# Performance work log

Hardware: AMD Instinct MI355X
Metric: run time of the kernel (lower is better)

## Reference

```python
import jax, jax.numpy as jnp
import numpy as np

WS = 7            # window size
NH = 8            # num heads
C = 128           # hidden size
HS = C // NH      # head size = 16


def _rel_index(ws):
    # Swin-style relative position index for a ws x ws window -> [N, N]
    coords = np.stack(np.meshgrid(np.arange(ws), np.arange(ws), indexing='ij'), 0).reshape(2, -1)
    rel = coords[:, :, None] - coords[:, None, :] + (ws - 1)  # [2, N, N] in [0, 2ws-2]
    return jnp.asarray(rel[0] * (2 * ws - 1) + rel[1])        # [N, N] in [0, (2ws-1)^2)


def setup_inputs() -> dict:
    key = jax.random.key(0)
    ks = jax.random.split(key, 6)
    B, H, W = 16, 112, 112
    s = 0.02
    return {
        'x': jax.random.normal(ks[0], (B, H, W, C), jnp.float32),
        'w_q': jax.random.normal(ks[1], (C, C), jnp.float32) * s,
        'w_k': jax.random.normal(ks[2], (C, C), jnp.float32) * s,
        'w_v': jax.random.normal(ks[3], (C, C), jnp.float32) * s,
        'w_o': jax.random.normal(ks[4], (C, C), jnp.float32) * s,
        'b_o': jnp.zeros((C,), jnp.float32),
        'rel_bias': jax.random.normal(ks[5], ((2 * WS - 1) ** 2, NH), jnp.float32) * s,
    }


def reference(x, w_q, w_k, w_v, w_o, b_o, rel_bias):
    B, H, W, Cc = x.shape
    ws = WS
    N = ws * ws
    # window partition: [B,H,W,C] -> [B*nH*nW, ws*ws, C]
    xw = x.reshape(B, H // ws, ws, W // ws, ws, Cc)
    xw = xw.transpose(0, 1, 3, 2, 4, 5).reshape(-1, N, Cc)
    # qkv projections, split heads: [nW, N, C] -> [nW, NH, N, HS]
    scale = HS ** -0.5
    q = (xw @ w_q).reshape(-1, N, NH, HS).transpose(0, 2, 1, 3) * scale
    k = (xw @ w_k).reshape(-1, N, NH, HS).transpose(0, 2, 1, 3)
    v = (xw @ w_v).reshape(-1, N, NH, HS).transpose(0, 2, 1, 3)
    # attention logits + relative position bias
    attn = jnp.einsum('bhnd,bhmd->bhnm', q, k)
    bias = rel_bias[_rel_index(ws)].transpose(2, 0, 1)  # [NH, N, N]
    attn = jax.nn.softmax(attn + bias[None], axis=-1)
    o = jnp.einsum('bhnm,bhmd->bhnd', attn, v)
    o = o.transpose(0, 2, 1, 3).reshape(-1, N, Cc)
    o = o @ w_o + b_o
    # stitch windows back: [B*nH*nW, N, C] -> [B, H, W, C]
    o = o.reshape(B, H // ws, W // ws, ws, ws, Cc)
    return o.transpose(0, 1, 3, 2, 4, 5).reshape(B, H, W, Cc)
```

## Files before the change

kernel.cpp:

```cpp
#include <hip/hip_runtime.h>

typedef __bf16 bf16_t;
typedef __attribute__((ext_vector_type(8))) __bf16 bf16x8;
typedef __attribute__((ext_vector_type(4))) __bf16 bf16x4;
typedef __attribute__((ext_vector_type(4))) float f32x4;
typedef __attribute__((ext_vector_type(4))) short short4v;

#if __has_builtin(__builtin_amdgcn_mfma_f32_16x16x16bf16_1k)
#define HAVE_MFMA16 1
#else
#define HAVE_MFMA16 0
#endif

#if __has_builtin(__builtin_amdgcn_exp2f)
#define EXP2(x) __builtin_amdgcn_exp2f(x)
#else
#define EXP2(x) exp2f(x)
#endif

#define LDS_XW 0
#define LDS_O  0


__device__ __forceinline__ f32x4 mfma16(bf16x4 a, bf16x4 b, f32x4 c) {
#if HAVE_MFMA16
    return __builtin_amdgcn_mfma_f32_16x16x16bf16_1k(
        __builtin_bit_cast(short4v, a), __builtin_bit_cast(short4v, b), c, 0, 0, 0);
#else
    bf16x8 a8, b8;
#pragma unroll
    for (int j = 0; j < 8; ++j) { a8[j] = (bf16_t)0.0f; b8[j] = (bf16_t)0.0f; }
#pragma unroll
    for (int j = 0; j < 4; ++j) { a8[j] = a[j]; b8[j] = b[j]; }
    return __builtin_amdgcn_mfma_f32_16x16x32_bf16(a8, b8, c, 0, 0, 0);
#endif
}

__global__ void repack_kernel(const float* __restrict__ wq, const float* __restrict__ wk,
                              const float* __restrict__ wv, const float* __restrict__ wo,
                              const float* __restrict__ rel_bias, bf16_t* __restrict__ ws)
{
    const float LOG2E = 1.44269504088896f;
    int idx = blockIdx.x * 256 + threadIdx.x;
    if (idx < 65536) {
        int mat = idx >> 14;
        int r = idx & 16383;
        int j = r & 7, l = (r >> 3) & 63, nt = (r >> 9) & 7, ks = r >> 12;
        int k = ks * 32 + (l >> 4) * 8 + j;
        int n = nt * 16 + (l & 15);
        const float* w = (mat == 0) ? wq : (mat == 1) ? wk : (mat == 2) ? wv : wo;
        float v = w[k * 128 + n];
        if (mat == 0) v *= 0.25f * LOG2E;
        ws[idx] = (bf16_t)v;
    } else if (idx < 98304) {
        int r = idx - 65536;
        int h = r >> 12, m = (r >> 6) & 63, n = r & 63;
        float v = -14427.0f;
        if (m < 49 && n < 49) {
            int im = m / 7, jm = m % 7, in_ = n / 7, jn = n % 7;
            v = rel_bias[((im - in_ + 6) * 13 + (jm - jn + 6)) * 8 + h] * LOG2E;
        }
        ((float*)(ws + 65536))[r] = v;
    }
}

__global__ __launch_bounds__(512, 4)
void win_attn_kernel(const float* __restrict__ x, const float* __restrict__ b_o,
                     const bf16_t* __restrict__ wpack, float* __restrict__ out)
{
    __shared__ __align__(16) unsigned char smem[12800];
    int* offTab = (int*)(smem + 12544);
    const float* biasT = (const float*)(wpack + 65536);
    const int tid = threadIdx.x;
    const int blk = blockIdx.x;
    const int b  = blk >> 8;
    const int wh = (blk >> 4) & 15;
    const int ww = blk & 15;
    const int w  = tid >> 6;
    const int lane = tid & 63;
    const int c  = lane & 15;
    const int hi = lane >> 4;
    const f32x4 fzero = {0.f, 0.f, 0.f, 0.f};

    if (tid < 64) {
        int mm = (tid < 49) ? tid : 48;
        int i = mm / 7, j = mm - 7 * i;
        offTab[tid] = ((b * 112 + wh * 7 + i) * 112 + ww * 7 + j) * 128;
    }
#pragma unroll
    for (int it = 0; it < 4; ++it) {
        int idx = tid + it * 512;
        if (idx < 1568) {
            int m  = idx >> 5;
            int c4 = idx & 31;
            int i = m / 7, j = m - 7 * i;
            float4 v = *(const float4*)(x + ((b * 112 + wh * 7 + i) * 112 + ww * 7 + j) * 128 + c4 * 4);
            bf16x4 bv;
            bv[0] = (bf16_t)v.x; bv[1] = (bf16_t)v.y; bv[2] = (bf16_t)v.z; bv[3] = (bf16_t)v.w;
            int ch = (c4 >> 1) ^ (m & 7);
            *(bf16x4*)(smem + LDS_XW + m * 256 + ch * 16 + (c4 & 1) * 8) = bv;
        }
    }
    __syncthreads();

    bf16x4 qreg[4], kreg[4], vreg[4];
#pragma unroll
    for (int nt = 0; nt < 4; ++nt) {
        int row = nt * 16 + c;
        int rowc = (row < 49) ? row : 48;
        const unsigned char* xbase = smem + LDS_XW + rowc * 256;
        int rsw = rowc & 7;
        bf16x8 xf[4];
#pragma unroll
        for (int ks = 0; ks < 4; ++ks)
            xf[ks] = *(const bf16x8*)(xbase + (((4 * ks + hi) ^ rsw) << 4));
        f32x4 aq = fzero, ak = fzero, av = fzero;
#pragma unroll
        for (int ks = 0; ks < 4; ++ks) {
            bf16x8 w0 = *(const bf16x8*)(wpack + 0 * 16384 + ((ks * 8 + w) * 64 + lane) * 8);
            bf16x8 w1 = *(const bf16x8*)(wpack + 1 * 16384 + ((ks * 8 + w) * 64 + lane) * 8);
            bf16x8 w2 = *(const bf16x8*)(wpack + 2 * 16384 + ((ks * 8 + w) * 64 + lane) * 8);
            aq = __builtin_amdgcn_mfma_f32_16x16x32_bf16(w0, xf[ks], aq, 0, 0, 0);
            ak = __builtin_amdgcn_mfma_f32_16x16x32_bf16(w1, xf[ks], ak, 0, 0, 0);
            av = __builtin_amdgcn_mfma_f32_16x16x32_bf16(xf[ks], w2, av, 0, 0, 0);
        }
        bf16x4 q, k, vv;
#pragma unroll
        for (int r = 0; r < 4; ++r) {
            q[r]  = (bf16_t)aq[r];
            k[r]  = (bf16_t)ak[r];
            vv[r] = (bf16_t)av[r];
        }
        qreg[nt] = q; kreg[nt] = k; vreg[nt] = vv;
    }
    __syncthreads();

    const int col = 16 * w + c;
    const int colhi = col >> 3;
    const int collo = (col & 7) * 2;
    int chO[4];
#pragma unroll
    for (int r = 0; r < 4; ++r)
        chO[r] = (colhi ^ ((4 * hi + r) & 7)) * 16 + collo;
#pragma unroll
    for (int mt = 0; mt < 4; ++mt) {
        int m = mt * 16 + c;
        f32x4 st[4];
#pragma unroll
        for (int nt = 0; nt < 4; ++nt) {
            f32x4 bb = *(const f32x4*)(biasT + (w * 64 + m) * 64 + nt * 16 + 4 * hi);
            st[nt] = mfma16(kreg[nt], qreg[mt], bb);
        }
        float sum = 0.f;
#pragma unroll
        for (int nt = 0; nt < 4; ++nt)
#pragma unroll
            for (int r = 0; r < 4; ++r) {
                float p = EXP2(st[nt][r]);
                st[nt][r] = p;
                sum += p;
            }
        sum += __shfl_xor(sum, 16);
        sum += __shfl_xor(sum, 32);
        float inv = 1.f / sum;
        f32x4 oacc = fzero;
#pragma unroll
        for (int nt = 0; nt < 4; ++nt) {
            bf16x4 pv;
#pragma unroll
            for (int r = 0; r < 4; ++r) pv[r] = (bf16_t)st[nt][r];
            oacc = mfma16(pv, vreg[nt], oacc);
        }
#pragma unroll
        for (int r = 0; r < 4; ++r) {
            float invr = __shfl(inv, 4 * hi + r);
            int row = mt * 16 + hi * 4 + r;
            if (row < 49)
                *(bf16_t*)(smem + LDS_O + row * 256 + chO[r]) = (bf16_t)(oacc[r] * invr);
        }
    }
    __syncthreads();

    float bb = b_o[col];
#pragma unroll
    for (int mt = 0; mt < 4; ++mt) {
        int row = mt * 16 + c;
        int rowc = (row < 49) ? row : 48;
        f32x4 acc = fzero;
#pragma unroll
        for (int ks = 0; ks < 4; ++ks) {
            int ch = (4 * ks + hi) ^ (rowc & 7);
            bf16x8 a  = *(const bf16x8*)(smem + LDS_O + rowc * 256 + ch * 16);
            bf16x8 w0 = *(const bf16x8*)(wpack + 3 * 16384 + ((ks * 8 + w) * 64 + lane) * 8);
            acc = __builtin_amdgcn_mfma_f32_16x16x32_bf16(a, w0, acc, 0, 0, 0);
        }
        int4 o4 = *(const int4*)(offTab + mt * 16 + 4 * hi);
        int offv[4] = {o4.x, o4.y, o4.z, o4.w};
#pragma unroll
        for (int r = 0; r < 4; ++r) {
            int m = mt * 16 + hi * 4 + r;
            if (m < 49)
                out[offv[r] + col] = acc[r] + bb;
        }
    }
}

extern "C" void kernel_launch(void* const* d_in, const int* in_sizes, int n_in,
                              void* d_out, int out_size, void* d_ws, size_t ws_size,
                              hipStream_t stream) {
    const float* x   = (const float*)d_in[0];
    const float* wq  = (const float*)d_in[1];
    const float* wk  = (const float*)d_in[2];
    const float* wvp = (const float*)d_in[3];
    const float* wo  = (const float*)d_in[4];
    const float* bo  = (const float*)d_in[5];
    const float* rb  = (const float*)d_in[6];
    bf16_t* wpack = (bf16_t*)d_ws;

    repack_kernel<<<384, 256, 0, stream>>>(wq, wk, wvp, wo, rb, wpack);
    win_attn_kernel<<<4096, 512, 0, stream>>>(x, bo, wpack, (float*)d_out);
}
```

Baseline: 102.7 us.

## Process two adjacent windows per block to amortize weight loads

Each block now handles two horizontally adjacent windows, loading both into LDS and running projection, attention and output projection for each in sequence. The grid is halved and the output-projection weights are hoisted into registers once per block. The aim is to amortize per-block overheads and weight fetches across two windows. In exchange it doubles LDS use and raises register pressure because two sets of q/k/v fragments are live, which could reduce occupancy under launch_bounds(512,4).

```diff
diff --git a/kernel.cpp b/kernel.cpp
--- a/kernel.cpp
+++ b/kernel.cpp
@@ -18,8 +18,6 @@
 #define EXP2(x) exp2f(x)
 #endif
 
-#define LDS_XW 0
-#define LDS_O  0
 
 
 __device__ __forceinline__ f32x4 mfma16(bf16x4 a, bf16x4 b, f32x4 c) {
@@ -68,71 +66,77 @@
 void win_attn_kernel(const float* __restrict__ x, const float* __restrict__ b_o,
                      const bf16_t* __restrict__ wpack, float* __restrict__ out)
 {
-    __shared__ __align__(16) unsigned char smem[12800];
-    int* offTab = (int*)(smem + 12544);
+    __shared__ __align__(16) unsigned char smem[25600];
+    int* offTab = (int*)(smem + 25088);
     const float* biasT = (const float*)(wpack + 65536);
     const int tid = threadIdx.x;
-    const int blk = blockIdx.x;
-    const int b  = blk >> 8;
-    const int wh = (blk >> 4) & 15;
-    const int ww = blk & 15;
-    const int w  = tid >> 6;
+    const int blk2 = blockIdx.x;
+    const int widA = blk2 * 2;
+    const int b   = widA >> 8;
+    const int wh  = (widA >> 4) & 15;
+    const int wwA = widA & 15;
+    const int w   = tid >> 6;
     const int lane = tid & 63;
     const int c  = lane & 15;
     const int hi = lane >> 4;
     const f32x4 fzero = {0.f, 0.f, 0.f, 0.f};
 
-    if (tid < 64) {
-        int mm = (tid < 49) ? tid : 48;
+    if (tid < 128) {
+        int win = tid >> 6;
+        int mm = tid & 63; if (mm > 48) mm = 48;
         int i = mm / 7, j = mm - 7 * i;
-        offTab[tid] = ((b * 112 + wh * 7 + i) * 112 + ww * 7 + j) * 128;
-    }
-#pragma unroll
-    for (int it = 0; it < 4; ++it) {
+        offTab[tid] = ((b * 112 + wh * 7 + i) * 112 + (wwA + win) * 7 + j) * 128;
+    }
+#pragma unroll
+    for (int it = 0; it < 7; ++it) {
         int idx = tid + it * 512;
-        if (idx < 1568) {
-            int m  = idx >> 5;
-            int c4 = idx & 31;
+        if (idx < 3136) {
+            int win = (idx >= 1568) ? 1 : 0;
+            int t = idx - win * 1568;
+            int m  = t >> 5;
+            int c4 = t & 31;
             int i = m / 7, j = m - 7 * i;
-            float4 v = *(const float4*)(x + ((b * 112 + wh * 7 + i) * 112 + ww * 7 + j) * 128 + c4 * 4);
+            float4 v = *(const float4*)(x + ((b * 112 + wh * 7 + i) * 112 + (wwA + win) * 7 + j) * 128 + c4 * 4);
             bf16x4 bv;
             bv[0] = (bf16_t)v.x; bv[1] = (bf16_t)v.y; bv[2] = (bf16_t)v.z; bv[3] = (bf16_t)v.w;
             int ch = (c4 >> 1) ^ (m & 7);
-            *(bf16x4*)(smem + LDS_XW + m * 256 + ch * 16 + (c4 & 1) * 8) = bv;
+            *(bf16x4*)(smem + win * 12544 + m * 256 + ch * 16 + (c4 & 1) * 8) = bv;
         }
     }
     __syncthreads();
 
-    bf16x4 qreg[4], kreg[4], vreg[4];
-#pragma unroll
-    for (int nt = 0; nt < 4; ++nt) {
-        int row = nt * 16 + c;
-        int rowc = (row < 49) ? row : 48;
-        const unsigned char* xbase = smem + LDS_XW + rowc * 256;
-        int rsw = rowc & 7;
-        bf16x8 xf[4];
-#pragma unroll
-        for (int ks = 0; ks < 4; ++ks)
-            xf[ks] = *(const bf16x8*)(xbase + (((4 * ks + hi) ^ rsw) << 4));
-        f32x4 aq = fzero, ak = fzero, av = fzero;
-#pragma unroll
-        for (int ks = 0; ks < 4; ++ks) {
-            bf16x8 w0 = *(const bf16x8*)(wpack + 0 * 16384 + ((ks * 8 + w) * 64 + lane) * 8);
-            bf16x8 w1 = *(const bf16x8*)(wpack + 1 * 16384 + ((ks * 8 + w) * 64 + lane) * 8);
-            bf16x8 w2 = *(const bf16x8*)(wpack + 2 * 16384 + ((ks * 8 + w) * 64 + lane) * 8);
-            aq = __builtin_amdgcn_mfma_f32_16x16x32_bf16(w0, xf[ks], aq, 0, 0, 0);
-            ak = __builtin_amdgcn_mfma_f32_16x16x32_bf16(w1, xf[ks], ak, 0, 0, 0);
-            av = __builtin_amdgcn_mfma_f32_16x16x32_bf16(xf[ks], w2, av, 0, 0, 0);
-        }
-        bf16x4 q, k, vv;
-#pragma unroll
-        for (int r = 0; r < 4; ++r) {
-            q[r]  = (bf16_t)aq[r];
-            k[r]  = (bf16_t)ak[r];
-            vv[r] = (bf16_t)av[r];
-        }
-        qreg[nt] = q; kreg[nt] = k; vreg[nt] = vv;
-    }
+    auto proj = [&](int base, bf16x4 (&qr)[4], bf16x4 (&kr)[4], bf16x4 (&vr)[4]) {
+#pragma unroll
+        for (int nt = 0; nt < 4; ++nt) {
+            int row = nt * 16 + c;
+            int rowc = (row < 49) ? row : 48;
+            const unsigned char* xbase = smem + base + rowc * 256;
+            int rsw = rowc & 7;
+            bf16x8 xf[4];
+#pragma unroll
+            for (int ks = 0; ks < 4; ++ks)
+                xf[ks] = *(const bf16x8*)(xbase + (((4 * ks + hi) ^ rsw) << 4));
+            f32x4 aq = fzero, ak = fzero, av = fzero;
+#pragma unroll
+            for (int ks = 0; ks < 4; ++ks) {
+                bf16x8 w0 = *(const bf16x8*)(wpack + 0 * 16384 + ((ks * 8 + w) * 64 + lane) * 8);
+                bf16x8 w1 = *(const bf16x8*)(wpack + 1 * 16384 + ((ks * 8 + w) * 64 + lane) * 8);
+                bf16x8 w2 = *(const bf16x8*)(wpack + 2 * 16384 + ((ks * 8 + w) * 64 + lane) * 8);
+                aq = __builtin_amdgcn_mfma_f32_16x16x32_bf16(w0, xf[ks], aq, 0, 0, 0);
+                ak = __builtin_amdgcn_mfma_f32_16x16x32_bf16(w1, xf[ks], ak, 0, 0, 0);
+                av = __builtin_amdgcn_mfma_f32_16x16x32_bf16(xf[ks], w2, av, 0, 0, 0);
+            }
+#pragma unroll
+            for (int r = 0; r < 4; ++r) {
+                qr[nt][r] = (bf16_t)aq[r];
+                kr[nt][r] = (bf16_t)ak[r];
+                vr[nt][r] = (bf16_t)av[r];
+            }
+        }
+    };
+    bf16x4 qregA[4], kregA[4], vregA[4], qregB[4], kregB[4], vregB[4];
+    proj(0,     qregA, kregA, vregA);
+    proj(12544, qregB, kregB, vregB);
     __syncthreads();
 
     const int col = 16 * w + c;
@@ -142,65 +146,78 @@
 #pragma unroll
     for (int r = 0; r < 4; ++r)
         chO[r] = (colhi ^ ((4 * hi + r) & 7)) * 16 + collo;
-#pragma unroll
-    for (int mt = 0; mt < 4; ++mt) {
-        int m = mt * 16 + c;
-        f32x4 st[4];
-#pragma unroll
-        for (int nt = 0; nt < 4; ++nt) {
-            f32x4 bb = *(const f32x4*)(biasT + (w * 64 + m) * 64 + nt * 16 + 4 * hi);
-            st[nt] = mfma16(kreg[nt], qreg[mt], bb);
-        }
-        float sum = 0.f;
-#pragma unroll
-        for (int nt = 0; nt < 4; ++nt)
+
+    auto attn = [&](int base, bf16x4 (&qr)[4], bf16x4 (&kr)[4], bf16x4 (&vr)[4]) {
+#pragma unroll
+        for (int mt = 0; mt < 4; ++mt) {
+            int m = mt * 16 + c;
+            f32x4 st[4];
+#pragma unroll
+            for (int nt = 0; nt < 4; ++nt) {
+                f32x4 bb = *(const f32x4*)(biasT + (w * 64 + m) * 64 + nt * 16 + 4 * hi);
+                st[nt] = mfma16(kr[nt], qr[mt], bb);
+            }
+            float sum = 0.f;
+#pragma unroll
+            for (int nt = 0; nt < 4; ++nt)
+#pragma unroll
+                for (int r = 0; r < 4; ++r) {
+                    float p = EXP2(st[nt][r]);
+                    st[nt][r] = p;
+                    sum += p;
+                }
+            sum += __shfl_xor(sum, 16);
+            sum += __shfl_xor(sum, 32);
+            float inv = 1.f / sum;
+            f32x4 oacc = fzero;
+#pragma unroll
+            for (int nt = 0; nt < 4; ++nt) {
+                bf16x4 pv;
+#pragma unroll
+                for (int r = 0; r < 4; ++r) pv[r] = (bf16_t)st[nt][r];
+                oacc = mfma16(pv, vr[nt], oacc);
+            }
 #pragma unroll
             for (int r = 0; r < 4; ++r) {
-                float p = EXP2(st[nt][r]);
-                st[nt][r] = p;
-                sum += p;
-            }
-        sum += __shfl_xor(sum, 16);
-        sum += __shfl_xor(sum, 32);
-        float inv = 1.f / sum;
-        f32x4 oacc = fzero;
-#pragma unroll
-        for (int nt = 0; nt < 4; ++nt) {
-            bf16x4 pv;
-#pragma unroll
-            for (int r = 0; r < 4; ++r) pv[r] = (bf16_t)st[nt][r];
-            oacc = mfma16(pv, vreg[nt], oacc);
-        }
-#pragma unroll
-        for (int r = 0; r < 4; ++r) {
-            float invr = __shfl(inv, 4 * hi + r);
-            int row = mt * 16 + hi * 4 + r;
-            if (row < 49)
-                *(bf16_t*)(smem + LDS_O + row * 256 + chO[r]) = (bf16_t)(oacc[r] * invr);
-        }
-    }
+                float invr = __shfl(inv, 4 * hi + r);
+                int row = mt * 16 + hi * 4 + r;
+                if (row < 49)
+                    *(bf16_t*)(smem + base + row * 256 + chO[r]) = (bf16_t)(oacc[r] * invr);
+            }
+        }
+    };
+    attn(0,     qregA, kregA, vregA);
+    attn(12544, qregB, kregB, vregB);
     __syncthreads();
 
+    bf16x8 wof[4];
+#pragma unroll
+    for (int ks = 0; ks < 4; ++ks)
+        wof[ks] = *(const bf16x8*)(wpack + 3 * 16384 + ((ks * 8 + w) * 64 + lane) * 8);
     float bb = b_o[col];
 #pragma unroll
-    for (int mt = 0; mt < 4; ++mt) {
-        int row = mt * 16 + c;
-        int rowc = (row < 49) ? row : 48;
-        f32x4 acc = fzero;
-#pragma unroll
-        for (int ks = 0; ks < 4; ++ks) {
-            int ch = (4 * ks + hi) ^ (rowc & 7);
-            bf16x8 a  = *(const bf16x8*)(smem + LDS_O + rowc * 256 + ch * 16);
-            bf16x8 w0 = *(const bf16x8*)(wpack + 3 * 16384 + ((ks * 8 + w) * 64 + lane) * 8);
-            acc = __builtin_amdgcn_mfma_f32_16x16x32_bf16(a, w0, acc, 0, 0, 0);
-        }
-        int4 o4 = *(const int4*)(offTab + mt * 16 + 4 * hi);
-        int offv[4] = {o4.x, o4.y, o4.z, o4.w};
-#pragma unroll
-        for (int r = 0; r < 4; ++r) {
-            int m = mt * 16 + hi * 4 + r;
-            if (m < 49)
-                out[offv[r] + col] = acc[r] + bb;
+    for (int win = 0; win < 2; ++win) {
+        const unsigned char* obase = smem + win * 12544;
+        const int* otab = offTab + win * 64;
+#pragma unroll
+        for (int mt = 0; mt < 4; ++mt) {
+            int row = mt * 16 + c;
+            int rowc = (row < 49) ? row : 48;
+            int rsw = rowc & 7;
+            f32x4 acc = fzero;
+#pragma unroll
+            for (int ks = 0; ks < 4; ++ks) {
+                bf16x8 a = *(const bf16x8*)(obase + rowc * 256 + (((4 * ks + hi) ^ rsw) << 4));
+                acc = __builtin_amdgcn_mfma_f32_16x16x32_bf16(a, wof[ks], acc, 0, 0, 0);
+            }
+            int4 o4 = *(const int4*)(otab + mt * 16 + 4 * hi);
+            int offv[4] = {o4.x, o4.y, o4.z, o4.w};
+#pragma unroll
+            for (int r = 0; r < 4; ++r) {
+                int m = mt * 16 + hi * 4 + r;
+                if (m < 49)
+                    out[offv[r] + col] = acc[r] + bb;
+            }
         }
     }
 }
@@ -218,5 +235,5 @@
     bf16_t* wpack = (bf16_t*)d_ws;
 
     repack_kernel<<<384, 256, 0, stream>>>(wq, wk, wvp, wo, rb, wpack);
-    win_attn_kernel<<<4096, 512, 0, stream>>>(x, bo, wpack, (float*)d_out);
-}
+    win_attn_kernel<<<2048, 512, 0, stream>>>(x, bo, wpack, (float*)d_out);
+}
```

Result: slower. 142.6 us (+38.8%).
